# Performance work log

Measured on AMD Instinct MI355X. Metric: run time of the kernel, lower is better.

## Reference

```python
import jax, jax.numpy as jnp
import numpy as np

B, S, R, D, A, P = 64, 128, 8, 10000, 10, 256


def setup_inputs() -> dict:
    key = jax.random.key(0)
    ks = jax.random.split(key, 7)
    return {
        "atom_hvs": jax.random.normal(ks[0], (A, D), jnp.float32),
        "pos_hvs": jax.random.normal(ks[1], (S, D), jnp.float32),
        "closure_tag": jax.random.normal(ks[2], (D,), jnp.float32),
        "W": jax.random.normal(ks[3], (P, D), jnp.float32) / np.float32(np.sqrt(D)),
        "b": jax.random.normal(ks[4], (P,), jnp.float32) * 0.01,
        "token_mask": jnp.ones((B, S), jnp.float32),
        "ring_mask": jnp.ones((B, R), jnp.float32),
        "atom_idx": jax.random.randint(ks[5], (B, S), 0, A),
        "ring_pos": jax.random.randint(ks[6], (B, R, 2), 0, S),
    }


def reference(atom_hvs, pos_hvs, closure_tag, W, b, token_mask, ring_mask, atom_idx, ring_pos):
    # HRR bind = circular convolution -> pointwise multiply in rFFT domain.
    # Bundle = sum; by linearity we sum in the frequency domain and do a
    # single irfft per molecule (same math as per-token conv + add).
    d = atom_hvs.shape[-1]
    Fa = jnp.fft.rfft(atom_hvs, axis=-1)          # [A, F]
    Fp = jnp.fft.rfft(pos_hvs, axis=-1)           # [S, F]
    Fc = jnp.fft.rfft(closure_tag)                # [F]

    s = atom_idx.shape[1]
    tok = Fa[atom_idx] * Fp[None, :s, :]          # [B, S, F] gather+bind
    freq = jnp.sum(token_mask[..., None] * tok, axis=1)   # [B, F] bundle

    ring = Fp[ring_pos[..., 0]] * Fp[ring_pos[..., 1]] * Fc  # [B, R, F]
    freq = freq + jnp.sum(ring_mask[..., None] * ring, axis=1)

    mol_hv = jnp.fft.irfft(freq, n=d, axis=-1)    # [B, D]
    return mol_hv @ W.T + b                       # [B, proj_dim]
```

## Files before the change

kernel.cpp:

```cpp
#include <hip/hip_runtime.h>

#define PI2 6.28318530717958647692f

#define NSIG 139
#define FS   5120

__global__ __launch_bounds__(256) void k_fwd(
                     const float* __restrict__ atom, const float* __restrict__ pos,
                     const float* __restrict__ clo, float2* __restrict__ spec) {
  __shared__ float xs[5000];
  unsigned sig = blockIdx.x, q = blockIdx.y;
  unsigned k1base = q * 10u;
  unsigned nk1 = (k1base + 10u <= 51u) ? 10u : (51u - k1base);
  const float* xb = (sig < 128u) ? (pos + sig * 10000u)
                   : ((sig < 138u) ? (atom + (sig - 128u) * 10000u) : clo);
  int tid = threadIdx.x;
  unsigned ntile1 = nk1 * 25u;
  unsigned k1l = tid / 25u, n2 = (tid % 25u) * 4u;
  bool have = (unsigned)tid < ntile1;
  unsigned k1 = k1base + k1l;
  float cth, sth;
  __sincosf(PI2 * (float)k1 * 0.01f, &sth, &cth);
  float c = 1.0f, s = 0.0f;
  float ar[4] = {}, as[4] = {};

  for (int h = 0; h < 2; ++h) {
    for (int i = tid; i < 1250; i += 256)
      *(float4*)(xs + 4 * i) = *(const float4*)(xb + h * 5000 + 4 * i);
    __syncthreads();
    if (have) {
#pragma unroll 5
      for (int n1l = 0; n1l < 50; ++n1l) {
        const float4 xv = *(const float4*)(xs + n1l * 100 + n2);
        ar[0] += xv.x * c; as[0] += xv.x * s;
        ar[1] += xv.y * c; as[1] += xv.y * s;
        ar[2] += xv.z * c; as[2] += xv.z * s;
        ar[3] += xv.w * c; as[3] += xv.w * s;
        float cn = c * cth - s * sth;
        float sn = s * cth + c * sth;
        c = cn; s = sn;
      }
    }
    __syncthreads();
  }

  if (have) {
    unsigned rb = (100u - k1) % 100u;
    float resA[8], resB[8];
#pragma unroll
    for (int j = 0; j < 4; ++j) {
      float swA, cwA, swB, cwB;
      __sincosf(PI2 * (float)((n2 + j) * k1) * 1e-4f, &swA, &cwA);
      __sincosf(PI2 * (float)((n2 + j) * rb) * 1e-4f, &swB, &cwB);
      resA[2 * j + 0] = ar[j] * cwA - as[j] * swA;
      resA[2 * j + 1] = -(as[j] * cwA + ar[j] * swA);
      resB[2 * j + 0] = ar[j] * cwB + as[j] * swB;
      resB[2 * j + 1] = as[j] * cwB - ar[j] * swB;
    }
    float* pA = xs + k1l * 200u + n2 * 2u;
    float* pB = xs + (nk1 + k1l) * 200u + n2 * 2u;
    *(float4*)(pA + 0) = make_float4(resA[0], resA[1], resA[2], resA[3]);
    *(float4*)(pA + 4) = make_float4(resA[4], resA[5], resA[6], resA[7]);
    *(float4*)(pB + 0) = make_float4(resB[0], resB[1], resB[2], resB[3]);
    *(float4*)(pB + 4) = make_float4(resB[4], resB[5], resB[6], resB[7]);
  }
  __syncthreads();

  unsigned nrow = 2u * nk1;
  unsigned ntile3 = nrow * 26u;
  for (unsigned t = tid; t < ntile3; t += 256u) {
    unsigned lr = t / 26u, k2 = (t % 26u) * 2u;
    unsigned gk1 = (lr < nk1) ? (k1base + lr) : ((100u - (k1base + (lr - nk1))) % 100u);
    const float* brow = xs + lr * 200u;
    float cthA, sthA, cthB, sthB;
    __sincosf(PI2 * (float)k2 * 0.01f, &sthA, &cthA);
    __sincosf(PI2 * (float)(k2 + 1) * 0.01f, &sthB, &cthB);
    float cA = 1.0f, sA = 0.0f, cB = 1.0f, sB = 0.0f;
    float reA = 0.f, imA = 0.f, reB = 0.f, imB = 0.f;
#pragma unroll 4
    for (int n2i = 0; n2i < 100; n2i += 2) {
      const float4 b0 = *(const float4*)(brow + 2 * n2i);
      reA += b0.x * cA + b0.y * sA;  imA += b0.y * cA - b0.x * sA;
      reB += b0.x * cB + b0.y * sB;  imB += b0.y * cB - b0.x * sB;
      float cA1 = cA * cthA - sA * sthA, sA1 = sA * cthA + cA * sthA;
      float cB1 = cB * cthB - sB * sthB, sB1 = sB * cthB + cB * sthB;
      reA += b0.z * cA1 + b0.w * sA1;  imA += b0.w * cA1 - b0.z * sA1;
      reB += b0.z * cB1 + b0.w * sB1;  imB += b0.w * cB1 - b0.z * sB1;
      cA = cA1 * cthA - sA1 * sthA; sA = sA1 * cthA + cA1 * sthA;
      cB = cB1 * cthB - sB1 * sthB; sB = sB1 * cthB + cB1 * sthB;
    }
    unsigned kA = gk1 + 100u * k2;
    unsigned kB = gk1 + 100u * (k2 + 1);
    if (kA <= 5000u) spec[sig * FS + kA] = make_float2(reA, imA);
    if (kB <= 5000u) spec[sig * FS + kB] = make_float2(reB, imB);
  }
}

__global__ void k_mix(const float2* __restrict__ spec,
                      const float* __restrict__ tmask, const float* __restrict__ rmask,
                      const int* __restrict__ aidx, const int* __restrict__ rpos,
                      float2* __restrict__ G) {
  __shared__ float2 FaS[10][256];
  __shared__ float2 FcS[256];
  __shared__ float tmS[2][128];
  __shared__ int   aiS[2][128];
  __shared__ float rmS[2][8];
  __shared__ int   rpS[2][8][2];
  int tid = threadIdx.x;
  int k = blockIdx.x * 256 + tid;
  int kc = k > 5000 ? 5000 : k;
  int b0 = blockIdx.y * 2;
#pragma unroll
  for (int a = 0; a < 10; ++a) FaS[a][tid] = spec[(128 + a) * FS + kc];
  FcS[tid] = spec[138 * FS + kc];
  for (int i = tid; i < 2 * 128; i += 256) {
    int bb = i >> 7, ss = i & 127;
    tmS[bb][ss] = tmask[(b0 + bb) * 128 + ss];
    aiS[bb][ss] = aidx[(b0 + bb) * 128 + ss];
  }
  if (tid < 16) {
    int bb = tid >> 3, rr = tid & 7;
    rmS[bb][rr] = rmask[(b0 + bb) * 8 + rr];
    rpS[bb][rr][0] = rpos[((b0 + bb) * 8 + rr) * 2 + 0];
    rpS[bb][rr][1] = rpos[((b0 + bb) * 8 + rr) * 2 + 1];
  }
  __syncthreads();
  float fr[2] = {}, fi[2] = {};
#pragma unroll 8
  for (int s = 0; s < 128; ++s) {
    float2 fp = spec[s * FS + kc];
#pragma unroll
    for (int b = 0; b < 2; ++b) {
      int a = aiS[b][s];
      float tm = tmS[b][s];
      float2 fa = FaS[a][tid];
      float tr = fa.x * fp.x - fa.y * fp.y;
      float ti = fa.x * fp.y + fa.y * fp.x;
      fr[b] += tm * tr;
      fi[b] += tm * ti;
    }
  }
  float2 fc = FcS[tid];
#pragma unroll
  for (int r = 0; r < 8; ++r) {
#pragma unroll
    for (int b = 0; b < 2; ++b) {
      int p0 = rpS[b][r][0], p1 = rpS[b][r][1];
      float rm = rmS[b][r];
      float2 f0 = spec[p0 * FS + kc];
      float2 f1 = spec[p1 * FS + kc];
      float tr = f0.x * f1.x - f0.y * f1.y;
      float ti = f0.x * f1.y + f0.y * f1.x;
      float ur = tr * fc.x - ti * fc.y;
      float ui = tr * fc.y + ti * fc.x;
      fr[b] += rm * ur;
      fi[b] += rm * ui;
    }
  }
  if (k <= 5000) {
#pragma unroll
    for (int b = 0; b < 2; ++b) {
      float fib = (k == 0 || k == 5000) ? 0.0f : fi[b];
      G[(size_t)(b0 + b) * 10000 + k] = make_float2(fr[b], fib);
      if (k >= 1 && k <= 4999)
        G[(size_t)(b0 + b) * 10000 + (10000 - k)] = make_float2(fr[b], -fib);
    }
  }
}

__global__ __launch_bounds__(256) void k_i1(const float2* __restrict__ G,
                                            float2* __restrict__ Bi) {
  __shared__ float gs[2600];
  unsigned sig = blockIdx.x;
  const float* gp = (const float*)(G + sig * 10000u);
  int tid = threadIdx.x;
  unsigned t = blockIdx.y * 256u + tid;
  bool have = t < 2600u;
  unsigned m1 = t / 26u, n2 = (t % 26u) * 2u;
  float cth, sth;
  __sincosf(PI2 * (float)m1 * 0.01f, &sth, &cth);
  float reA = 0.f, imA = 0.f, reB = 0.f, imB = 0.f;

  for (int h = 0; h < 4; ++h) {
    if (h) __syncthreads();
    for (int i = tid; i < 650; i += 256) {
      int row = i / 26, c4 = i % 26;
      *(float4*)(gs + row * 104 + c4 * 4) =
          *(const float4*)(gp + (h * 25 + row) * 200 + c4 * 4);
    }
    __syncthreads();
    if (have) {
      unsigned ph = (m1 * (unsigned)h) & 3u;
      float c = (ph == 0u) ? 1.0f : (ph == 2u) ? -1.0f : 0.0f;
      float s = (ph == 1u) ? 1.0f : (ph == 3u) ? -1.0f : 0.0f;
#pragma unroll 5
      for (int n1l = 0; n1l < 25; ++n1l) {
        const float4 gv = *(const float4*)(gs + n1l * 104 + n2 * 2);
        reA += gv.x * c - gv.y * s;  imA += gv.y * c + gv.x * s;
        reB += gv.z * c - gv.w * s;  imB += gv.w * c + gv.z * s;
        float cn = c * cth - s * sth;
        float sn = s * cth + c * sth;
        c = cn; s = sn;
      }
    }
  }
  if (have) {
    float w0 = (n2 == 0u || n2 == 50u) ? 0.5f : 1.0f;
    float w1 = (n2 == 50u) ? 0.0f : 1.0f;
    float sw0, cw0, sw1, cw1;
    __sincosf(PI2 * (float)(n2 * m1) * 1e-4f, &sw0, &cw0);
    __sincosf(PI2 * (float)((n2 + 1u) * m1) * 1e-4f, &sw1, &cw1);
    float4 outv;
    outv.x = (reA * cw0 - imA * sw0) * w0;
    outv.y = (imA * cw0 + reA * sw0) * w0;
    outv.z = (reB * cw1 - imB * sw1) * w1;
    outv.w = (imB * cw1 + reB * sw1) * w1;
    *(float4*)((float*)Bi + (sig * 5200u + m1 * 52u + n2) * 2) = outv;
  }
}

__global__ __launch_bounds__(256) void k_i2(const float2* __restrict__ Bi,
                                            float* __restrict__ mol) {
  __shared__ float bs[2600];
  unsigned sig = blockIdx.x, q = blockIdx.y;
  int tid = threadIdx.x;
  const float* bp = (const float*)Bi + sig * 10400u + q * 2600u;
  for (int i = tid; i < 650; i += 256)
    *(float4*)(bs + 4 * i) = *(const float4*)(bp + 4 * i);
  __syncthreads();
  unsigned t = blockIdx.z * 256u + tid;
  if (t >= 1250u) return;
  unsigned m1l = t / 50u;
  unsigned m2 = (t % 50u) * 2u;
  const float* b0 = bs + m1l * 104u;
  float cthA, sthA, cthB, sthB;
  __sincosf(PI2 * (float)m2 * 0.01f, &sthA, &cthA);
  __sincosf(PI2 * (float)(m2 + 1u) * 0.01f, &sthB, &cthB);
  float cA = 1.0f, sA = 0.0f, cB = 1.0f, sB = 0.0f;
  float r0 = 0.f, r1 = 0.f;
#pragma unroll 4
  for (int jj = 0; jj < 26; ++jj) {
    int n2i = 2 * jj;
    const float4 v0 = *(const float4*)(b0 + 2 * n2i);
    r0 += v0.x * cA - v0.y * sA;
    r1 += v0.x * cB - v0.y * sB;
    float cA1 = cA * cthA - sA * sthA, sA1 = sA * cthA + cA * sthA;
    float cB1 = cB * cthB - sB * sthB, sB1 = sB * cthB + cB * sthB;
    r0 += v0.z * cA1 - v0.w * sA1;
    r1 += v0.z * cB1 - v0.w * sB1;
    cA = cA1 * cthA - sA1 * sthA; sA = sA1 * cthA + cA1 * sthA;
    cB = cB1 * cthB - sB1 * sthB; sB = sB1 * cthB + cB1 * sthB;
  }
  unsigned m1 = q * 25u + m1l;
  mol[sig * 10000u + m1 + 100u * m2] = r0 * 2e-4f;
  mol[sig * 10000u + m1 + 100u * (m2 + 1u)] = r1 * 2e-4f;
}

__global__ __launch_bounds__(256) void k_proj(const float* __restrict__ mol,
                                              const float* __restrict__ W,
                                              float* __restrict__ part) {
  __shared__ float molS[40 * 64];
  int tid = threadIdx.x;
  int d0 = blockIdx.x * 40;
  for (int i = tid; i < 40 * 64; i += 256)
    molS[i] = mol[(size_t)(i & 63) * 10000 + d0 + (i >> 6)];
  __syncthreads();
  int p0 = (tid & 63) * 4;
  int bh = (tid >> 6) * 16;
  float acc[4][16] = {};
  const float* w0 = W + (size_t)(p0 + 0) * 10000 + d0;
  const float* w1 = W + (size_t)(p0 + 1) * 10000 + d0;
  const float* w2 = W + (size_t)(p0 + 2) * 10000 + d0;
  const float* w3 = W + (size_t)(p0 + 3) * 10000 + d0;
#pragma unroll 4
  for (int dl = 0; dl < 40; ++dl) {
    const float wv[4] = {w0[dl], w1[dl], w2[dl], w3[dl]};
    const float4* m4 = (const float4*)(molS + dl * 64 + bh);
#pragma unroll
    for (int q = 0; q < 4; ++q) {
      float4 mv = m4[q];
#pragma unroll
      for (int pp = 0; pp < 4; ++pp) {
        acc[pp][4 * q + 0] += wv[pp] * mv.x;
        acc[pp][4 * q + 1] += wv[pp] * mv.y;
        acc[pp][4 * q + 2] += wv[pp] * mv.z;
        acc[pp][4 * q + 3] += wv[pp] * mv.w;
      }
    }
  }
#pragma unroll
  for (int b = 0; b < 16; ++b) {
    float4 v = make_float4(acc[0][b], acc[1][b], acc[2][b], acc[3][b]);
    *(float4*)(part + (size_t)blockIdx.x * 16384 + (bh + b) * 256 + p0) = v;
  }
}

__global__ __launch_bounds__(64) void k_red(const float* __restrict__ part,
                                            const float* __restrict__ bias,
                                            float* __restrict__ out) {
  int tid = threadIdx.x;
  int b = blockIdx.x;
  int p = blockIdx.y * 64 + tid;
  float acc = bias[p];
#pragma unroll 8
  for (int ch = 0; ch < 250; ++ch)
    acc += part[(size_t)ch * 16384 + b * 256 + p];
  out[b * 256 + p] = acc;
}

extern "C" void kernel_launch(void* const* d_in, const int* in_sizes, int n_in,
                              void* d_out, int out_size, void* d_ws, size_t ws_size,
                              hipStream_t stream) {
  const float* atom  = (const float*)d_in[0];
  const float* pos   = (const float*)d_in[1];
  const float* clo   = (const float*)d_in[2];
  const float* W     = (const float*)d_in[3];
  const float* bias  = (const float*)d_in[4];
  const float* tmask = (const float*)d_in[5];
  const float* rmask = (const float*)d_in[6];
  const int*   aidx  = (const int*)d_in[7];
  const int*   rpos  = (const int*)d_in[8];
  float* out = (float*)d_out;

  char* ws = (char*)d_ws;
  size_t off = 0;
  auto alloc = [&](size_t n) { off = (off + 255) & ~(size_t)255; size_t o = off; off += n; return o; };
  char* regA   = ws + alloc(16777216);
  float2* Bi   = (float2*)regA;
  float*  part = (float*)regA;
  float2* spec = (float2*)(ws + alloc((size_t)NSIG * FS * 8));
  float2* G    = (float2*)(ws + alloc((size_t)64 * 10000 * 8));
  float*  mol  = (float*)(ws + alloc((size_t)64 * 10000 * 4));

  k_fwd<<<dim3(NSIG, 6), dim3(256), 0, stream>>>(atom, pos, clo, spec);
  k_mix<<<dim3(20, 32), dim3(256), 0, stream>>>(spec, tmask, rmask, aidx, rpos, G);
  k_i1<<<dim3(64, 11), dim3(256), 0, stream>>>(G, Bi);
  k_i2<<<dim3(64, 4, 5), dim3(256), 0, stream>>>(Bi, mol);
  k_proj<<<dim3(250), dim3(256), 0, stream>>>(mol, W, part);
  k_red<<<dim3(64, 4), dim3(64), 0, stream>>>(part, bias, out);
}
```

Measured before the change: 191.1 us.

## Split mix, projection and reduction work across more threads per block

k_mix now covers 128 frequencies per block with two thread halves, each summing half of the sequence positions and half of the rings for 4 molecules. The halves are combined through shared memory, which doubles reuse of each pos-spectrum load across molecules. k_proj moves to 512 threads with 2 outputs per thread instead of 4, and k_red splits the 250-chunk reduction over 4 thread groups with a shared-memory combine. This raises thread-level parallelism and latency hiding, at the cost of an extra sync and lower per-thread register reuse.

```diff
diff --git a/kernel.cpp b/kernel.cpp
--- a/kernel.cpp
+++ b/kernel.cpp
@@ -96,74 +96,84 @@
   }
 }
 
-__global__ void k_mix(const float2* __restrict__ spec,
+__global__ __launch_bounds__(256) void k_mix(const float2* __restrict__ spec,
                       const float* __restrict__ tmask, const float* __restrict__ rmask,
                       const int* __restrict__ aidx, const int* __restrict__ rpos,
                       float2* __restrict__ G) {
-  __shared__ float2 FaS[10][256];
-  __shared__ float2 FcS[256];
-  __shared__ float tmS[2][128];
-  __shared__ int   aiS[2][128];
-  __shared__ float rmS[2][8];
-  __shared__ int   rpS[2][8][2];
-  int tid = threadIdx.x;
-  int k = blockIdx.x * 256 + tid;
+  __shared__ float2 FaS[10][128];
+  __shared__ float2 FcS[128];
+  __shared__ float tmS[4][128];
+  __shared__ int   aiS[4][128];
+  __shared__ float rmS[4][8];
+  __shared__ int   rpS[4][8][2];
+  __shared__ float2 red[2][4][128];
+  int tid = threadIdx.x;
+  int kl = tid & 127, half = tid >> 7;
+  int k = blockIdx.x * 128 + kl;
   int kc = k > 5000 ? 5000 : k;
-  int b0 = blockIdx.y * 2;
-#pragma unroll
-  for (int a = 0; a < 10; ++a) FaS[a][tid] = spec[(128 + a) * FS + kc];
-  FcS[tid] = spec[138 * FS + kc];
-  for (int i = tid; i < 2 * 128; i += 256) {
+  int b0 = blockIdx.y * 4;
+  for (int i = tid; i < 10 * 128; i += 256) {
+    int a = i >> 7, kk = i & 127;
+    int kg = blockIdx.x * 128 + kk; if (kg > 5000) kg = 5000;
+    FaS[a][kk] = spec[(128 + a) * FS + kg];
+  }
+  if (tid < 128) FcS[tid] = spec[138 * FS + kc];
+  for (int i = tid; i < 4 * 128; i += 256) {
     int bb = i >> 7, ss = i & 127;
     tmS[bb][ss] = tmask[(b0 + bb) * 128 + ss];
     aiS[bb][ss] = aidx[(b0 + bb) * 128 + ss];
   }
-  if (tid < 16) {
+  if (tid < 32) {
     int bb = tid >> 3, rr = tid & 7;
     rmS[bb][rr] = rmask[(b0 + bb) * 8 + rr];
     rpS[bb][rr][0] = rpos[((b0 + bb) * 8 + rr) * 2 + 0];
     rpS[bb][rr][1] = rpos[((b0 + bb) * 8 + rr) * 2 + 1];
   }
   __syncthreads();
-  float fr[2] = {}, fi[2] = {};
+  float fr[4] = {}, fi[4] = {};
+  int sbase = half * 64;
 #pragma unroll 8
-  for (int s = 0; s < 128; ++s) {
+  for (int si = 0; si < 64; ++si) {
+    int s = sbase + si;
     float2 fp = spec[s * FS + kc];
 #pragma unroll
-    for (int b = 0; b < 2; ++b) {
+    for (int b = 0; b < 4; ++b) {
       int a = aiS[b][s];
       float tm = tmS[b][s];
-      float2 fa = FaS[a][tid];
-      float tr = fa.x * fp.x - fa.y * fp.y;
-      float ti = fa.x * fp.y + fa.y * fp.x;
-      fr[b] += tm * tr;
-      fi[b] += tm * ti;
-    }
-  }
-  float2 fc = FcS[tid];
-#pragma unroll
-  for (int r = 0; r < 8; ++r) {
-#pragma unroll
-    for (int b = 0; b < 2; ++b) {
+      float2 fa = FaS[a][kl];
+      fr[b] += tm * (fa.x * fp.x - fa.y * fp.y);
+      fi[b] += tm * (fa.x * fp.y + fa.y * fp.x);
+    }
+  }
+  float2 fc = FcS[kl];
+#pragma unroll
+  for (int rr = 0; rr < 4; ++rr) {
+    int r = half * 4 + rr;
+#pragma unroll
+    for (int b = 0; b < 4; ++b) {
       int p0 = rpS[b][r][0], p1 = rpS[b][r][1];
       float rm = rmS[b][r];
       float2 f0 = spec[p0 * FS + kc];
       float2 f1 = spec[p1 * FS + kc];
       float tr = f0.x * f1.x - f0.y * f1.y;
       float ti = f0.x * f1.y + f0.y * f1.x;
-      float ur = tr * fc.x - ti * fc.y;
-      float ui = tr * fc.y + ti * fc.x;
-      fr[b] += rm * ur;
-      fi[b] += rm * ui;
-    }
-  }
+      fr[b] += rm * (tr * fc.x - ti * fc.y);
+      fi[b] += rm * (tr * fc.y + ti * fc.x);
+    }
+  }
+#pragma unroll
+  for (int b = 0; b < 4; ++b) red[half][b][kl] = make_float2(fr[b], fi[b]);
+  __syncthreads();
   if (k <= 5000) {
 #pragma unroll
-    for (int b = 0; b < 2; ++b) {
-      float fib = (k == 0 || k == 5000) ? 0.0f : fi[b];
-      G[(size_t)(b0 + b) * 10000 + k] = make_float2(fr[b], fib);
+    for (int j = 0; j < 2; ++j) {
+      int b = half + 2 * j;
+      float R = red[0][b][kl].x + red[1][b][kl].x;
+      float I = red[0][b][kl].y + red[1][b][kl].y;
+      if (k == 0 || k == 5000) I = 0.0f;
+      G[(size_t)(b0 + b) * 10000 + k] = make_float2(R, I);
       if (k >= 1 && k <= 4999)
-        G[(size_t)(b0 + b) * 10000 + (10000 - k)] = make_float2(fr[b], -fib);
+        G[(size_t)(b0 + b) * 10000 + (10000 - k)] = make_float2(R, -I);
     }
   }
 }
@@ -256,56 +266,55 @@
   mol[sig * 10000u + m1 + 100u * (m2 + 1u)] = r1 * 2e-4f;
 }
 
-__global__ __launch_bounds__(256) void k_proj(const float* __restrict__ mol,
+__global__ __launch_bounds__(512) void k_proj(const float* __restrict__ mol,
                                               const float* __restrict__ W,
                                               float* __restrict__ part) {
   __shared__ float molS[40 * 64];
   int tid = threadIdx.x;
   int d0 = blockIdx.x * 40;
-  for (int i = tid; i < 40 * 64; i += 256)
+  for (int i = tid; i < 40 * 64; i += 512)
     molS[i] = mol[(size_t)(i & 63) * 10000 + d0 + (i >> 6)];
   __syncthreads();
-  int p0 = (tid & 63) * 4;
-  int bh = (tid >> 6) * 16;
-  float acc[4][16] = {};
+  int p0 = (tid & 127) * 2;
+  int bh = (tid >> 7) * 16;
+  float acc[2][16] = {};
   const float* w0 = W + (size_t)(p0 + 0) * 10000 + d0;
   const float* w1 = W + (size_t)(p0 + 1) * 10000 + d0;
-  const float* w2 = W + (size_t)(p0 + 2) * 10000 + d0;
-  const float* w3 = W + (size_t)(p0 + 3) * 10000 + d0;
 #pragma unroll 4
   for (int dl = 0; dl < 40; ++dl) {
-    const float wv[4] = {w0[dl], w1[dl], w2[dl], w3[dl]};
+    const float wv0 = w0[dl], wv1 = w1[dl];
     const float4* m4 = (const float4*)(molS + dl * 64 + bh);
 #pragma unroll
     for (int q = 0; q < 4; ++q) {
       float4 mv = m4[q];
-#pragma unroll
-      for (int pp = 0; pp < 4; ++pp) {
-        acc[pp][4 * q + 0] += wv[pp] * mv.x;
-        acc[pp][4 * q + 1] += wv[pp] * mv.y;
-        acc[pp][4 * q + 2] += wv[pp] * mv.z;
-        acc[pp][4 * q + 3] += wv[pp] * mv.w;
-      }
-    }
-  }
-#pragma unroll
-  for (int b = 0; b < 16; ++b) {
-    float4 v = make_float4(acc[0][b], acc[1][b], acc[2][b], acc[3][b]);
-    *(float4*)(part + (size_t)blockIdx.x * 16384 + (bh + b) * 256 + p0) = v;
-  }
-}
-
-__global__ __launch_bounds__(64) void k_red(const float* __restrict__ part,
-                                            const float* __restrict__ bias,
-                                            float* __restrict__ out) {
-  int tid = threadIdx.x;
+      acc[0][4 * q + 0] += wv0 * mv.x;  acc[1][4 * q + 0] += wv1 * mv.x;
+      acc[0][4 * q + 1] += wv0 * mv.y;  acc[1][4 * q + 1] += wv1 * mv.y;
+      acc[0][4 * q + 2] += wv0 * mv.z;  acc[1][4 * q + 2] += wv1 * mv.z;
+      acc[0][4 * q + 3] += wv0 * mv.w;  acc[1][4 * q + 3] += wv1 * mv.w;
+    }
+  }
+#pragma unroll
+  for (int b = 0; b < 16; ++b)
+    *(float2*)(part + (size_t)blockIdx.x * 16384 + (bh + b) * 256 + p0) =
+        make_float2(acc[0][b], acc[1][b]);
+}
+
+__global__ __launch_bounds__(256) void k_red(const float* __restrict__ part,
+                                             const float* __restrict__ bias,
+                                             float* __restrict__ out) {
+  __shared__ float red[4][64];
+  int tid = threadIdx.x;
+  int pl = tid & 63, cg = tid >> 6;
   int b = blockIdx.x;
-  int p = blockIdx.y * 64 + tid;
-  float acc = bias[p];
+  int p = blockIdx.y * 64 + pl;
+  float acc = 0.0f;
 #pragma unroll 8
-  for (int ch = 0; ch < 250; ++ch)
+  for (int ch = cg; ch < 250; ch += 4)
     acc += part[(size_t)ch * 16384 + b * 256 + p];
-  out[b * 256 + p] = acc;
+  red[cg][pl] = acc;
+  __syncthreads();
+  if (tid < 64)
+    out[b * 256 + p] = red[0][pl] + red[1][pl] + red[2][pl] + red[3][pl] + bias[p];
 }
 
 extern "C" void kernel_launch(void* const* d_in, const int* in_sizes, int n_in,
@@ -333,9 +342,9 @@
   float*  mol  = (float*)(ws + alloc((size_t)64 * 10000 * 4));
 
   k_fwd<<<dim3(NSIG, 6), dim3(256), 0, stream>>>(atom, pos, clo, spec);
-  k_mix<<<dim3(20, 32), dim3(256), 0, stream>>>(spec, tmask, rmask, aidx, rpos, G);
+  k_mix<<<dim3(40, 16), dim3(256), 0, stream>>>(spec, tmask, rmask, aidx, rpos, G);
   k_i1<<<dim3(64, 11), dim3(256), 0, stream>>>(G, Bi);
   k_i2<<<dim3(64, 4, 5), dim3(256), 0, stream>>>(Bi, mol);
-  k_proj<<<dim3(250), dim3(256), 0, stream>>>(mol, W, part);
-  k_red<<<dim3(64, 4), dim3(64), 0, stream>>>(part, bias, out);
-}
+  k_proj<<<dim3(250), dim3(512), 0, stream>>>(mol, W, part);
+  k_red<<<dim3(64, 4), dim3(256), 0, stream>>>(part, bias, out);
+}
```

Result: no change. 188.0 us (-1.6%).
